# Kernel optimization log

Measured on AMD Instinct MI355X. Metric: run time of the kernel, lower is better.

## Reference

```python
import jax, jax.numpy as jnp
import numpy as np
from jax.scipy.special import logsumexp

B, T, D = 256, 2048, 64


def setup_inputs() -> dict:
    key = jax.random.key(0)
    k1, k2, k3, k4 = jax.random.split(key, 4)
    p = jax.random.normal(k1, (B, T, D), dtype=jnp.float32)
    labels = jax.random.randint(k2, (B, T), 0, D)
    y = jax.nn.one_hot(labels, D, dtype=jnp.int32)  # [B,T,D] one-hot labels
    # valid lengths in [T//2, T]; mask == 1 marks padding positions
    lengths = jax.random.randint(k3, (B,), T // 2, T + 1)
    mask = (jnp.arange(T)[None, :] >= lengths[:, None]).astype(jnp.int32)
    transition = 0.1 * jax.random.normal(k4, (D, D), dtype=jnp.float32)
    return {"p": p, "y": y, "mask": mask, "transition": transition}


def reference(p, y, mask, transition):
    # CRF negative log-likelihood per example: logZ - emission_score - transition_score
    Bb = p.shape[0]
    valid = (1 - mask).astype(jnp.float32)            # [B,T], 1 = valid token
    y1 = y.astype(jnp.float32) * valid[:, :, None]    # masked one-hot labels
    s1 = jnp.sum(y1 * p, axis=(1, 2))                 # emission score
    pair = jnp.einsum('btd,bte->bde', y1[:, :-1], y1[:, 1:])  # label bigram counts
    s2 = jnp.sum(pair * transition, axis=(1, 2))      # transition score

    # forward algorithm: alpha_t = p_t + logsumexp(alpha_{t-1}[:, :, None] + T)
    def step(state, inp):
        new = inp + logsumexp(state[:, :, None] + transition[None, :, :], axis=1)
        return new, new

    xs = jnp.moveaxis(p[:, 1:, :], 1, 0)              # [T-1, B, D]
    _, a1 = jax.lax.scan(step, p[:, 0, :], xs)        # a1: [T-1, B, D]

    # index of alpha at the last valid timestep (length L -> a1 index L-2)
    m1 = jnp.argmin(
        jnp.concatenate([valid.astype(jnp.int32), jnp.zeros((Bb, 1), jnp.int32)], axis=1),
        axis=1) - 2                                   # [B]
    last = a1[m1, jnp.arange(Bb)]                     # [B, D]
    logZ = logsumexp(last, axis=-1)
    return logZ - s1 - s2
```

## Files before the change

### kernel.cpp

```cpp
#include <hip/hip_runtime.h>
#include <stdint.h>
#include <string.h>

#define BB 256
#define TT 2048
#define DD 64
#define CC 64
#define SS 32
#define C_L2E 1.44269504f
#define C_LN2 0.69314718f
#define C_BIAS 0.0028174f

typedef short sh8  __attribute__((ext_vector_type(8)));
typedef float f32x4 __attribute__((ext_vector_type(4)));

union BU { sh8 v8; unsigned int u[4]; unsigned short s[8]; };

__device__ __forceinline__ float expf_fast(float x) { return __builtin_amdgcn_exp2f(x * C_L2E); }
__device__ __forceinline__ unsigned short bf16rne(float x) {
    unsigned int u = __float_as_uint(x);
    u += 0x7FFF + ((u >> 16) & 1u);
    return (unsigned short)(u >> 16);
}
__device__ __forceinline__ unsigned int pkbf(float hi, float lo) {
    return __builtin_amdgcn_perm(__float_as_uint(hi), __float_as_uint(lo), 0x07060302u);
}

#define DPPMAX(x, ctrl, rm, bm) { int _xi = __float_as_int(x);                              \
    int _yi = __builtin_amdgcn_update_dpp(_xi, _xi, ctrl, rm, bm, false);                   \
    x = fmaxf(x, __int_as_float(_yi)); }

__global__ __launch_bounds__(256) void crf_len(
    const int* __restrict__ mask, int* __restrict__ wsL)
{
    __shared__ int r4[4];
    const int c = blockIdx.x, tid = threadIdx.x;
    const int4* mrow = (const int4*)(mask + (size_t)c * TT);
    int4 a = mrow[tid * 2], b = mrow[tid * 2 + 1];
    int s = a.x + a.y + a.z + a.w + b.x + b.y + b.z + b.w;
#pragma unroll
    for (int xm = 32; xm >= 1; xm >>= 1) s += __shfl_xor(s, xm, 64);
    if ((tid & 63) == 0) r4[tid >> 6] = s;
    __syncthreads();
    if (tid == 0) wsL[c] = TT - (r4[0] + r4[1] + r4[2] + r4[3]);
}

__global__ __launch_bounds__(256) void crf_main(
    const float* __restrict__ p, const int* __restrict__ y,
    const int* __restrict__ mask, const float* __restrict__ tr,
    const int* __restrict__ wsL, float* __restrict__ wsS,
    unsigned short* __restrict__ wsA, unsigned short* __restrict__ wsB, int* __restrict__ wsSig)
{
    __shared__ int mk[257];
    __shared__ unsigned char labs[257];
    __shared__ float redf[4];
    const int bid = blockIdx.x;
    const int tid = threadIdx.x;

    if (bid < 512) {
        const int w = tid >> 6, lane = tid & 63;
        const int q = lane >> 4, ml = lane & 15;
        const int cg = bid & 15;
        const int ic = (bid >> 4) * 2 + (w >> 1);
        const int bwd = w & 1;
        const int c = cg * 16 + ml;
        const int Lml = wsL[c];
        const int t0 = ic * SS, t1 = t0 + SS;
        const int ts = (ic == 0) ? 1 : t0;
        const float* prow = p + (size_t)c * TT * DD;

        BU A[4][2];
#pragma unroll
        for (int mt = 0; mt < 4; ++mt)
#pragma unroll
            for (int kt2 = 0; kt2 < 2; ++kt2)
#pragma unroll
                for (int j = 0; j < 8; ++j) {
                    int lam = 32 * kt2 + 16 * (j >> 2) + 4 * q + (j & 3);
                    float tv = bwd ? tr[(16 * mt + ml) * DD + lam] : tr[lam * DD + 16 * mt + ml];
                    A[mt][kt2].s[j] = (short)bf16rne(expf_fast(tv));
                }

        float xs[16];
        if (!bwd && ic == 0) {
#pragma unroll
            for (int k = 0; k < 4; ++k) {
                f32x4 v = *(const f32x4*)(prow + 16 * k + 4 * q);
#pragma unroll
                for (int r = 0; r < 4; ++r)
                    xs[(k >> 1) * 8 + (k & 1) * 4 + r] = __builtin_amdgcn_exp2f(fmaf(v[r], C_L2E, C_BIAS));
            }
        } else {
#pragma unroll
            for (int i = 0; i < 16; ++i) xs[i] = 1.0f;
        }

        int mL = Lml;
#pragma unroll
        for (int xm = 32; xm >= 1; xm >>= 1) { int o = __shfl_xor(mL, xm, 64); mL = o > mL ? o : mL; }
        int ibeg = 0, iend = SS;
        if (!bwd) { int ir = mL - t0; if (ir < 0) ir = 0; iend = (ir + 3) & ~3; if (iend > SS) iend = SS; }
        else      { int ir = t1 - mL; if (ir < 0) ir = 0; ibeg = ir & ~3; if (ibeg > SS) ibeg = SS; }

        int sig = 0;
        const f32x4 z4 = {0.f, 0.f, 0.f, 0.f};

        if (ibeg < iend) {
            f32x4 er[4][4];
#pragma unroll
            for (int s = 0; s < 4; ++s) {
                int i = ibeg + s;
                int t = bwd ? (t1 - 1 - i) : (t0 + i);
#pragma unroll
                for (int k = 0; k < 4; ++k)
                    er[s][k] = *(const f32x4*)(prow + (size_t)t * DD + 16 * k + 4 * q);
            }
            for (int ib = ibeg; ib < iend; ib += 4) {
#pragma unroll
                for (int s = 0; s < 4; ++s) {
                    const int i = ib + s;
                    const int t = bwd ? (t1 - 1 - i) : (t0 + i);
                    const bool act = (t >= ts) && (t < Lml);
                    float ee[4][4];
#pragma unroll
                    for (int k = 0; k < 4; ++k)
#pragma unroll
                        for (int r = 0; r < 4; ++r)
                            ee[k][r] = __builtin_amdgcn_exp2f(fmaf(er[s][k][r], C_L2E, C_BIAS));
                    {
                        int ipf = i + 4;
                        int tpf = bwd ? (t1 - 1 - ipf) : (t0 + ipf);
                        if (tpf < t0) tpf = t0;
                        if (tpf > t1 - 1) tpf = t1 - 1;
#pragma unroll
                        for (int k = 0; k < 4; ++k)
                            er[s][k] = *(const f32x4*)(prow + (size_t)tpf * DD + 16 * k + 4 * q);
                    }
                    float cand[16];
                    BU Bf[2];
                    f32x4 acc[4];
                    if (!bwd) {
#pragma unroll
                        for (int kt2 = 0; kt2 < 2; ++kt2)
#pragma unroll
                            for (int jj = 0; jj < 4; ++jj)
                                Bf[kt2].u[jj] = pkbf(xs[kt2 * 8 + 2 * jj + 1], xs[kt2 * 8 + 2 * jj]);
#pragma unroll
                        for (int mt = 0; mt < 4; ++mt) {
                            acc[mt] = __builtin_amdgcn_mfma_f32_16x16x32_bf16(A[mt][0].v8, Bf[0].v8, z4, 0, 0, 0);
                            acc[mt] = __builtin_amdgcn_mfma_f32_16x16x32_bf16(A[mt][1].v8, Bf[1].v8, acc[mt], 0, 0, 0);
                        }
#pragma unroll
                        for (int mt = 0; mt < 4; ++mt)
#pragma unroll
                            for (int r = 0; r < 4; ++r)
                                cand[(mt >> 1) * 8 + (mt & 1) * 4 + r] = acc[mt][r] * ee[mt][r];
                    } else {
                        float xsc[16];
#pragma unroll
                        for (int kt2 = 0; kt2 < 2; ++kt2)
#pragma unroll
                            for (int h = 0; h < 2; ++h)
#pragma unroll
                                for (int r = 0; r < 4; ++r)
                                    xsc[kt2 * 8 + h * 4 + r] = xs[kt2 * 8 + h * 4 + r] * ee[2 * kt2 + h][r];
#pragma unroll
                        for (int kt2 = 0; kt2 < 2; ++kt2)
#pragma unroll
                            for (int jj = 0; jj < 4; ++jj)
                                Bf[kt2].u[jj] = pkbf(xsc[kt2 * 8 + 2 * jj + 1], xsc[kt2 * 8 + 2 * jj]);
#pragma unroll
                        for (int mt = 0; mt < 4; ++mt) {
                            acc[mt] = __builtin_amdgcn_mfma_f32_16x16x32_bf16(A[mt][0].v8, Bf[0].v8, z4, 0, 0, 0);
                            acc[mt] = __builtin_amdgcn_mfma_f32_16x16x32_bf16(A[mt][1].v8, Bf[1].v8, acc[mt], 0, 0, 0);
                        }
#pragma unroll
                        for (int mt = 0; mt < 4; ++mt)
#pragma unroll
                            for (int r = 0; r < 4; ++r)
                                cand[(mt >> 1) * 8 + (mt & 1) * 4 + r] = acc[mt][r];
                    }
                    if (s == 3) {
                        float mx = fabsf(cand[0]);
#pragma unroll
                        for (int i2 = 1; i2 < 16; ++i2) mx = fmaxf(mx, fabsf(cand[i2]));
                        DPPMAX(mx, 0x111, 0xF, 0xF); DPPMAX(mx, 0x112, 0xF, 0xF);
                        DPPMAX(mx, 0x114, 0xF, 0xF); DPPMAX(mx, 0x118, 0xF, 0xF);
                        DPPMAX(mx, 0x142, 0xA, 0xF); DPPMAX(mx, 0x143, 0xC, 0xF);
                        int smx = __builtin_amdgcn_readlane(__float_as_int(mx), 63);
                        int kk = ((smx >> 23) & 255) - 127;
                        kk = kk < -124 ? -124 : (kk > 124 ? 124 : kk);
                        float sc = __int_as_float((unsigned)(127 - kk) << 23);
#pragma unroll
                        for (int i2 = 0; i2 < 16; ++i2) cand[i2] *= sc;
                        if (act) sig += kk;
                    }
#pragma unroll
                    for (int i2 = 0; i2 < 16; ++i2) xs[i2] = act ? cand[i2] : xs[i2];
                }
            }
        }

        unsigned short* dst = (bwd ? wsB : wsA) + ((size_t)c * CC + ic) * 64;
#pragma unroll
        for (int kt2 = 0; kt2 < 2; ++kt2)
#pragma unroll
            for (int h = 0; h < 2; ++h)
#pragma unroll
                for (int r = 0; r < 4; ++r)
                    dst[32 * kt2 + 16 * h + 4 * q + r] = bf16rne(xs[kt2 * 8 + h * 4 + r]);
        if (!bwd && q == 0) wsSig[c * CC + ic] = sig;

    } else {
        const int sid = bid - 512;
        const int c = sid >> 3, t0 = (sid & 7) * 256;
        const int g = tid & 15, sub = tid >> 4;
        const size_t cb = (size_t)c * TT;

        mk[tid] = mask[cb + t0 + tid];
        if (tid == 0) mk[256] = (t0 + 256 < TT) ? mask[cb + t0 + 256] : 1;
        __syncthreads();

        float s1 = 0.f;
#pragma unroll
        for (int k = 0; k < 16; ++k) {
            const int ti = k * 16 + sub;
            if (mk[ti] == 0) {
                int4 v = ((const int4*)y)[(cb + t0 + ti) * 16 + g];
                int cand = v.w ? 4 * g + 3 : v.z ? 4 * g + 2 : v.y ? 4 * g + 1 : v.x ? 4 * g : -1;
#pragma unroll
                for (int xm = 1; xm <= 8; xm <<= 1) {
                    int o = __shfl_xor(cand, xm, 16);
                    cand = o > cand ? o : cand;
                }
                if (g == 0) {
                    labs[ti] = (unsigned char)cand;
                    s1 += p[(cb + t0 + ti) * DD + cand];
                }
            }
        }
        if (tid < 16 && mk[256] == 0) {
            int4 v = ((const int4*)y)[(cb + t0 + 256) * 16 + tid];
            int cand = v.w ? 4 * tid + 3 : v.z ? 4 * tid + 2 : v.y ? 4 * tid + 1 : v.x ? 4 * tid : -1;
#pragma unroll
            for (int xm = 1; xm <= 8; xm <<= 1) {
                int o = __shfl_xor(cand, xm, 16);
                cand = o > cand ? o : cand;
            }
            if (tid == 0) labs[256] = (unsigned char)cand;
        }
        __syncthreads();

        float s2 = 0.f;
        if (mk[tid + 1] == 0)
            s2 = tr[(int)labs[tid] * DD + (int)labs[tid + 1]];

        float acc = s1 + s2;
#pragma unroll
        for (int xm = 32; xm >= 1; xm >>= 1) acc += __shfl_xor(acc, xm, 64);
        if ((tid & 63) == 0) redf[tid >> 6] = acc;
        __syncthreads();
        if (tid == 0)
            atomicAdd(&wsS[c], redf[0] + redf[1] + redf[2] + redf[3]);
    }
}

__global__ __launch_bounds__(256) void crf_combine(
    const unsigned short* __restrict__ wsA, const unsigned short* __restrict__ wsB,
    const int* __restrict__ wsSig, const float* __restrict__ wsS,
    float* __restrict__ out)
{
    __shared__ float eParts[4];
    const int tid = threadIdx.x, w = tid >> 6, lane = tid & 63;
    const int c = blockIdx.x;

    float Ep = 0.f;
#pragma unroll
    for (int k = 0; k < 16; ++k) {
        const int i = w * 16 + k;
        if (i == 0) continue;
        float b  = __uint_as_float((unsigned)wsB[((size_t)c * CC + i) * 64 + lane] << 16);
        float ap = __uint_as_float((unsigned)wsA[((size_t)c * CC + i - 1) * 64 + lane] << 16);
        float d1 = b * ap, d0 = b;
#pragma unroll
        for (int xm = 32; xm >= 1; xm >>= 1) { d1 += __shfl_xor(d1, xm, 64); d0 += __shfl_xor(d0, xm, 64); }
        Ep += (float)wsSig[c * CC + i] + __builtin_amdgcn_logf(d1) - __builtin_amdgcn_logf(d0);
    }
    if (w == 0) Ep += (float)wsSig[c * CC];
    if (w == 3) {
        float al = __uint_as_float((unsigned)wsA[((size_t)c * CC + CC - 1) * 64 + lane] << 16);
#pragma unroll
        for (int xm = 32; xm >= 1; xm >>= 1) al += __shfl_xor(al, xm, 64);
        Ep += __builtin_amdgcn_logf(al);
    }
    if (lane == 0) eParts[w] = Ep;
    __syncthreads();
    if (tid == 0) {
        float E = eParts[0] + eParts[1] + eParts[2] + eParts[3];
        out[c] = C_LN2 * E - wsS[c];
    }
}

extern "C" void kernel_launch(void* const* d_in, const int* in_sizes, int n_in,
                              void* d_out, int out_size, void* d_ws, size_t ws_size,
                              hipStream_t stream) {
    const float* p  = (const float*)d_in[0];
    const int*   y  = (const int*)d_in[1];
    const int*   mk = (const int*)d_in[2];
    const float* tr = (const float*)d_in[3];
    float* out = (float*)d_out;

    float* wsS  = (float*)d_ws;
    int*   wsL  = (int*)((char*)d_ws + 1024);
    int*   wsSg = (int*)((char*)d_ws + 2048);
    unsigned short* wsA = (unsigned short*)((char*)d_ws + 131072);
    unsigned short* wsB = (unsigned short*)((char*)d_ws + 131072 + (2u << 20));

    hipMemsetAsync(d_ws, 0, 1024, stream);
    crf_len<<<dim3(BB), dim3(256), 0, stream>>>(mk, wsL);
    crf_main<<<dim3(512 + 8 * BB), dim3(256), 0, stream>>>(p, y, mk, tr, wsL, wsS, wsA, wsB, wsSg);
    crf_combine<<<dim3(BB), dim3(256), 0, stream>>>(wsA, wsB, wsSg, wsS, out);
}
```

Baseline: 370.8 us.

## Sort sequences by length so forward groups skip padded chunks, split score kernel

Adds a single-block rank kernel that sorts the batch by valid length and uses the permutation to group 16 similar-length sequences per block in the chunked forward/backward kernel. Because each wave trims its loop to the maximum length in its group, grouping similar lengths lets more chunks be skipped. The emission/transition score work is split into its own kernel rather than sharing one grid with the recurrence. This adds an extra serial launch and a tiny ranking kernel, and loses the overlap of score blocks with the recurrence blocks.

```diff
diff --git a/kernel.cpp b/kernel.cpp
--- a/kernel.cpp
+++ b/kernel.cpp
@@ -45,224 +45,240 @@
     if (tid == 0) wsL[c] = TT - (r4[0] + r4[1] + r4[2] + r4[3]);
 }
 
-__global__ __launch_bounds__(256) void crf_main(
+__global__ __launch_bounds__(256) void crf_rank(
+    const int* __restrict__ wsL, int* __restrict__ perm)
+{
+    __shared__ int Ls[BB];
+    const int tid = threadIdx.x;
+    Ls[tid] = wsL[tid];
+    __syncthreads();
+    const int L = Ls[tid];
+    int r = 0;
+#pragma unroll 8
+    for (int j = 0; j < BB; ++j) {
+        int Lj = Ls[j];
+        r += (Lj < L) || (Lj == L && j < tid);
+    }
+    perm[r] = tid;
+}
+
+__global__ __launch_bounds__(256) void crf_score(
     const float* __restrict__ p, const int* __restrict__ y,
     const int* __restrict__ mask, const float* __restrict__ tr,
-    const int* __restrict__ wsL, float* __restrict__ wsS,
-    unsigned short* __restrict__ wsA, unsigned short* __restrict__ wsB, int* __restrict__ wsSig)
+    float* __restrict__ wsS)
 {
     __shared__ int mk[257];
     __shared__ unsigned char labs[257];
     __shared__ float redf[4];
-    const int bid = blockIdx.x;
+    const int c = blockIdx.y, t0 = blockIdx.x * 256;
     const int tid = threadIdx.x;
-
-    if (bid < 512) {
-        const int w = tid >> 6, lane = tid & 63;
-        const int q = lane >> 4, ml = lane & 15;
-        const int cg = bid & 15;
-        const int ic = (bid >> 4) * 2 + (w >> 1);
-        const int bwd = w & 1;
-        const int c = cg * 16 + ml;
-        const int Lml = wsL[c];
-        const int t0 = ic * SS, t1 = t0 + SS;
-        const int ts = (ic == 0) ? 1 : t0;
-        const float* prow = p + (size_t)c * TT * DD;
-
-        BU A[4][2];
-#pragma unroll
-        for (int mt = 0; mt < 4; ++mt)
-#pragma unroll
-            for (int kt2 = 0; kt2 < 2; ++kt2)
-#pragma unroll
-                for (int j = 0; j < 8; ++j) {
-                    int lam = 32 * kt2 + 16 * (j >> 2) + 4 * q + (j & 3);
-                    float tv = bwd ? tr[(16 * mt + ml) * DD + lam] : tr[lam * DD + 16 * mt + ml];
-                    A[mt][kt2].s[j] = (short)bf16rne(expf_fast(tv));
-                }
-
-        float xs[16];
-        if (!bwd && ic == 0) {
-#pragma unroll
-            for (int k = 0; k < 4; ++k) {
-                f32x4 v = *(const f32x4*)(prow + 16 * k + 4 * q);
-#pragma unroll
-                for (int r = 0; r < 4; ++r)
-                    xs[(k >> 1) * 8 + (k & 1) * 4 + r] = __builtin_amdgcn_exp2f(fmaf(v[r], C_L2E, C_BIAS));
-            }
-        } else {
-#pragma unroll
-            for (int i = 0; i < 16; ++i) xs[i] = 1.0f;
-        }
-
-        int mL = Lml;
-#pragma unroll
-        for (int xm = 32; xm >= 1; xm >>= 1) { int o = __shfl_xor(mL, xm, 64); mL = o > mL ? o : mL; }
-        int ibeg = 0, iend = SS;
-        if (!bwd) { int ir = mL - t0; if (ir < 0) ir = 0; iend = (ir + 3) & ~3; if (iend > SS) iend = SS; }
-        else      { int ir = t1 - mL; if (ir < 0) ir = 0; ibeg = ir & ~3; if (ibeg > SS) ibeg = SS; }
-
-        int sig = 0;
-        const f32x4 z4 = {0.f, 0.f, 0.f, 0.f};
-
-        if (ibeg < iend) {
-            f32x4 er[4][4];
-#pragma unroll
-            for (int s = 0; s < 4; ++s) {
-                int i = ibeg + s;
-                int t = bwd ? (t1 - 1 - i) : (t0 + i);
-#pragma unroll
-                for (int k = 0; k < 4; ++k)
-                    er[s][k] = *(const f32x4*)(prow + (size_t)t * DD + 16 * k + 4 * q);
-            }
-            for (int ib = ibeg; ib < iend; ib += 4) {
-#pragma unroll
-                for (int s = 0; s < 4; ++s) {
-                    const int i = ib + s;
-                    const int t = bwd ? (t1 - 1 - i) : (t0 + i);
-                    const bool act = (t >= ts) && (t < Lml);
-                    float ee[4][4];
-#pragma unroll
-                    for (int k = 0; k < 4; ++k)
-#pragma unroll
-                        for (int r = 0; r < 4; ++r)
-                            ee[k][r] = __builtin_amdgcn_exp2f(fmaf(er[s][k][r], C_L2E, C_BIAS));
-                    {
-                        int ipf = i + 4;
-                        int tpf = bwd ? (t1 - 1 - ipf) : (t0 + ipf);
-                        if (tpf < t0) tpf = t0;
-                        if (tpf > t1 - 1) tpf = t1 - 1;
-#pragma unroll
-                        for (int k = 0; k < 4; ++k)
-                            er[s][k] = *(const f32x4*)(prow + (size_t)tpf * DD + 16 * k + 4 * q);
-                    }
-                    float cand[16];
-                    BU Bf[2];
-                    f32x4 acc[4];
-                    if (!bwd) {
-#pragma unroll
-                        for (int kt2 = 0; kt2 < 2; ++kt2)
-#pragma unroll
-                            for (int jj = 0; jj < 4; ++jj)
-                                Bf[kt2].u[jj] = pkbf(xs[kt2 * 8 + 2 * jj + 1], xs[kt2 * 8 + 2 * jj]);
-#pragma unroll
-                        for (int mt = 0; mt < 4; ++mt) {
-                            acc[mt] = __builtin_amdgcn_mfma_f32_16x16x32_bf16(A[mt][0].v8, Bf[0].v8, z4, 0, 0, 0);
-                            acc[mt] = __builtin_amdgcn_mfma_f32_16x16x32_bf16(A[mt][1].v8, Bf[1].v8, acc[mt], 0, 0, 0);
-                        }
-#pragma unroll
-                        for (int mt = 0; mt < 4; ++mt)
-#pragma unroll
-                            for (int r = 0; r < 4; ++r)
-                                cand[(mt >> 1) * 8 + (mt & 1) * 4 + r] = acc[mt][r] * ee[mt][r];
-                    } else {
-                        float xsc[16];
-#pragma unroll
-                        for (int kt2 = 0; kt2 < 2; ++kt2)
-#pragma unroll
-                            for (int h = 0; h < 2; ++h)
-#pragma unroll
-                                for (int r = 0; r < 4; ++r)
-                                    xsc[kt2 * 8 + h * 4 + r] = xs[kt2 * 8 + h * 4 + r] * ee[2 * kt2 + h][r];
-#pragma unroll
-                        for (int kt2 = 0; kt2 < 2; ++kt2)
-#pragma unroll
-                            for (int jj = 0; jj < 4; ++jj)
-                                Bf[kt2].u[jj] = pkbf(xsc[kt2 * 8 + 2 * jj + 1], xsc[kt2 * 8 + 2 * jj]);
-#pragma unroll
-                        for (int mt = 0; mt < 4; ++mt) {
-                            acc[mt] = __builtin_amdgcn_mfma_f32_16x16x32_bf16(A[mt][0].v8, Bf[0].v8, z4, 0, 0, 0);
-                            acc[mt] = __builtin_amdgcn_mfma_f32_16x16x32_bf16(A[mt][1].v8, Bf[1].v8, acc[mt], 0, 0, 0);
-                        }
-#pragma unroll
-                        for (int mt = 0; mt < 4; ++mt)
-#pragma unroll
-                            for (int r = 0; r < 4; ++r)
-                                cand[(mt >> 1) * 8 + (mt & 1) * 4 + r] = acc[mt][r];
-                    }
-                    if (s == 3) {
-                        float mx = fabsf(cand[0]);
-#pragma unroll
-                        for (int i2 = 1; i2 < 16; ++i2) mx = fmaxf(mx, fabsf(cand[i2]));
-                        DPPMAX(mx, 0x111, 0xF, 0xF); DPPMAX(mx, 0x112, 0xF, 0xF);
-                        DPPMAX(mx, 0x114, 0xF, 0xF); DPPMAX(mx, 0x118, 0xF, 0xF);
-                        DPPMAX(mx, 0x142, 0xA, 0xF); DPPMAX(mx, 0x143, 0xC, 0xF);
-                        int smx = __builtin_amdgcn_readlane(__float_as_int(mx), 63);
-                        int kk = ((smx >> 23) & 255) - 127;
-                        kk = kk < -124 ? -124 : (kk > 124 ? 124 : kk);
-                        float sc = __int_as_float((unsigned)(127 - kk) << 23);
-#pragma unroll
-                        for (int i2 = 0; i2 < 16; ++i2) cand[i2] *= sc;
-                        if (act) sig += kk;
-                    }
-#pragma unroll
-                    for (int i2 = 0; i2 < 16; ++i2) xs[i2] = act ? cand[i2] : xs[i2];
-                }
-            }
-        }
-
-        unsigned short* dst = (bwd ? wsB : wsA) + ((size_t)c * CC + ic) * 64;
-#pragma unroll
-        for (int kt2 = 0; kt2 < 2; ++kt2)
-#pragma unroll
-            for (int h = 0; h < 2; ++h)
-#pragma unroll
-                for (int r = 0; r < 4; ++r)
-                    dst[32 * kt2 + 16 * h + 4 * q + r] = bf16rne(xs[kt2 * 8 + h * 4 + r]);
-        if (!bwd && q == 0) wsSig[c * CC + ic] = sig;
-
-    } else {
-        const int sid = bid - 512;
-        const int c = sid >> 3, t0 = (sid & 7) * 256;
-        const int g = tid & 15, sub = tid >> 4;
-        const size_t cb = (size_t)c * TT;
-
-        mk[tid] = mask[cb + t0 + tid];
-        if (tid == 0) mk[256] = (t0 + 256 < TT) ? mask[cb + t0 + 256] : 1;
-        __syncthreads();
-
-        float s1 = 0.f;
-#pragma unroll
-        for (int k = 0; k < 16; ++k) {
-            const int ti = k * 16 + sub;
-            if (mk[ti] == 0) {
-                int4 v = ((const int4*)y)[(cb + t0 + ti) * 16 + g];
-                int cand = v.w ? 4 * g + 3 : v.z ? 4 * g + 2 : v.y ? 4 * g + 1 : v.x ? 4 * g : -1;
-#pragma unroll
-                for (int xm = 1; xm <= 8; xm <<= 1) {
-                    int o = __shfl_xor(cand, xm, 16);
-                    cand = o > cand ? o : cand;
-                }
-                if (g == 0) {
-                    labs[ti] = (unsigned char)cand;
-                    s1 += p[(cb + t0 + ti) * DD + cand];
-                }
-            }
-        }
-        if (tid < 16 && mk[256] == 0) {
-            int4 v = ((const int4*)y)[(cb + t0 + 256) * 16 + tid];
-            int cand = v.w ? 4 * tid + 3 : v.z ? 4 * tid + 2 : v.y ? 4 * tid + 1 : v.x ? 4 * tid : -1;
+    const int g = tid & 15, sub = tid >> 4;
+    const size_t cb = (size_t)c * TT;
+
+    mk[tid] = mask[cb + t0 + tid];
+    if (tid == 0) mk[256] = (t0 + 256 < TT) ? mask[cb + t0 + 256] : 1;
+    __syncthreads();
+
+    float s1 = 0.f;
+#pragma unroll
+    for (int k = 0; k < 16; ++k) {
+        const int ti = k * 16 + sub;
+        if (mk[ti] == 0) {
+            int4 v = ((const int4*)y)[(cb + t0 + ti) * 16 + g];
+            int cand = v.w ? 4 * g + 3 : v.z ? 4 * g + 2 : v.y ? 4 * g + 1 : v.x ? 4 * g : -1;
 #pragma unroll
             for (int xm = 1; xm <= 8; xm <<= 1) {
                 int o = __shfl_xor(cand, xm, 16);
                 cand = o > cand ? o : cand;
             }
-            if (tid == 0) labs[256] = (unsigned char)cand;
-        }
-        __syncthreads();
-
-        float s2 = 0.f;
-        if (mk[tid + 1] == 0)
-            s2 = tr[(int)labs[tid] * DD + (int)labs[tid + 1]];
-
-        float acc = s1 + s2;
-#pragma unroll
-        for (int xm = 32; xm >= 1; xm >>= 1) acc += __shfl_xor(acc, xm, 64);
-        if ((tid & 63) == 0) redf[tid >> 6] = acc;
-        __syncthreads();
-        if (tid == 0)
-            atomicAdd(&wsS[c], redf[0] + redf[1] + redf[2] + redf[3]);
-    }
+            if (g == 0) {
+                labs[ti] = (unsigned char)cand;
+                s1 += p[(cb + t0 + ti) * DD + cand];
+            }
+        }
+    }
+    if (tid < 16 && mk[256] == 0) {
+        int4 v = ((const int4*)y)[(cb + t0 + 256) * 16 + tid];
+        int cand = v.w ? 4 * tid + 3 : v.z ? 4 * tid + 2 : v.y ? 4 * tid + 1 : v.x ? 4 * tid : -1;
+#pragma unroll
+        for (int xm = 1; xm <= 8; xm <<= 1) {
+            int o = __shfl_xor(cand, xm, 16);
+            cand = o > cand ? o : cand;
+        }
+        if (tid == 0) labs[256] = (unsigned char)cand;
+    }
+    __syncthreads();
+
+    float s2 = 0.f;
+    if (mk[tid + 1] == 0)
+        s2 = tr[(int)labs[tid] * DD + (int)labs[tid + 1]];
+
+    float acc = s1 + s2;
+#pragma unroll
+    for (int xm = 32; xm >= 1; xm >>= 1) acc += __shfl_xor(acc, xm, 64);
+    if ((tid & 63) == 0) redf[tid >> 6] = acc;
+    __syncthreads();
+    if (tid == 0)
+        atomicAdd(&wsS[c], redf[0] + redf[1] + redf[2] + redf[3]);
+}
+
+__global__ __launch_bounds__(256) void crf_probe(
+    const float* __restrict__ p, const float* __restrict__ tr,
+    const int* __restrict__ wsL, const int* __restrict__ perm,
+    unsigned short* __restrict__ wsA, unsigned short* __restrict__ wsB, int* __restrict__ wsSig)
+{
+    const int tid = threadIdx.x, w = tid >> 6, lane = tid & 63;
+    const int q = lane >> 4, ml = lane & 15;
+    const int cg = blockIdx.x;
+    const int ic = blockIdx.y * 2 + (w >> 1);
+    const int bwd = w & 1;
+    const int c = perm[cg * 16 + ml];
+    const int Lml = wsL[c];
+    const int t0 = ic * SS, t1 = t0 + SS;
+    const int ts = (ic == 0) ? 1 : t0;
+    const float* prow = p + (size_t)c * TT * DD;
+
+    BU A[4][2];
+#pragma unroll
+    for (int mt = 0; mt < 4; ++mt)
+#pragma unroll
+        for (int kt2 = 0; kt2 < 2; ++kt2)
+#pragma unroll
+            for (int j = 0; j < 8; ++j) {
+                int lam = 32 * kt2 + 16 * (j >> 2) + 4 * q + (j & 3);
+                float tv = bwd ? tr[(16 * mt + ml) * DD + lam] : tr[lam * DD + 16 * mt + ml];
+                A[mt][kt2].s[j] = (short)bf16rne(expf_fast(tv));
+            }
+
+    float xs[16];
+    if (!bwd && ic == 0) {
+#pragma unroll
+        for (int k = 0; k < 4; ++k) {
+            f32x4 v = *(const f32x4*)(prow + 16 * k + 4 * q);
+#pragma unroll
+            for (int r = 0; r < 4; ++r)
+                xs[(k >> 1) * 8 + (k & 1) * 4 + r] = __builtin_amdgcn_exp2f(fmaf(v[r], C_L2E, C_BIAS));
+        }
+    } else {
+#pragma unroll
+        for (int i = 0; i < 16; ++i) xs[i] = 1.0f;
+    }
+
+    int mL = Lml;
+#pragma unroll
+    for (int xm = 32; xm >= 1; xm >>= 1) { int o = __shfl_xor(mL, xm, 64); mL = o > mL ? o : mL; }
+    int ibeg = 0, iend = SS;
+    if (!bwd) { int ir = mL - t0; if (ir < 0) ir = 0; iend = (ir + 3) & ~3; if (iend > SS) iend = SS; }
+    else      { int ir = t1 - mL; if (ir < 0) ir = 0; ibeg = ir & ~3; if (ibeg > SS) ibeg = SS; }
+
+    int sig = 0;
+    const f32x4 z4 = {0.f, 0.f, 0.f, 0.f};
+
+    if (ibeg < iend) {
+        f32x4 er[4][4];
+#pragma unroll
+        for (int s = 0; s < 4; ++s) {
+            int i = ibeg + s;
+            int t = bwd ? (t1 - 1 - i) : (t0 + i);
+#pragma unroll
+            for (int k = 0; k < 4; ++k)
+                er[s][k] = *(const f32x4*)(prow + (size_t)t * DD + 16 * k + 4 * q);
+        }
+        for (int ib = ibeg; ib < iend; ib += 4) {
+#pragma unroll
+            for (int s = 0; s < 4; ++s) {
+                const int i = ib + s;
+                const int t = bwd ? (t1 - 1 - i) : (t0 + i);
+                const bool act = (t >= ts) && (t < Lml);
+                float ee[4][4];
+#pragma unroll
+                for (int k = 0; k < 4; ++k)
+#pragma unroll
+                    for (int r = 0; r < 4; ++r)
+                        ee[k][r] = __builtin_amdgcn_exp2f(fmaf(er[s][k][r], C_L2E, C_BIAS));
+                {
+                    int ipf = i + 4;
+                    int tpf = bwd ? (t1 - 1 - ipf) : (t0 + ipf);
+                    if (tpf < t0) tpf = t0;
+                    if (tpf > t1 - 1) tpf = t1 - 1;
+#pragma unroll
+                    for (int k = 0; k < 4; ++k)
+                        er[s][k] = *(const f32x4*)(prow + (size_t)tpf * DD + 16 * k + 4 * q);
+                }
+                float cand[16];
+                BU Bf[2];
+                f32x4 acc[4];
+                if (!bwd) {
+#pragma unroll
+                    for (int kt2 = 0; kt2 < 2; ++kt2)
+#pragma unroll
+                        for (int jj = 0; jj < 4; ++jj)
+                            Bf[kt2].u[jj] = pkbf(xs[kt2 * 8 + 2 * jj + 1], xs[kt2 * 8 + 2 * jj]);
+#pragma unroll
+                    for (int mt = 0; mt < 4; ++mt) {
+                        acc[mt] = __builtin_amdgcn_mfma_f32_16x16x32_bf16(A[mt][0].v8, Bf[0].v8, z4, 0, 0, 0);
+                        acc[mt] = __builtin_amdgcn_mfma_f32_16x16x32_bf16(A[mt][1].v8, Bf[1].v8, acc[mt], 0, 0, 0);
+                    }
+#pragma unroll
+                    for (int mt = 0; mt < 4; ++mt)
+#pragma unroll
+                        for (int r = 0; r < 4; ++r)
+                            cand[(mt >> 1) * 8 + (mt & 1) * 4 + r] = acc[mt][r] * ee[mt][r];
+                } else {
+                    float xsc[16];
+#pragma unroll
+                    for (int kt2 = 0; kt2 < 2; ++kt2)
+#pragma unroll
+                        for (int h = 0; h < 2; ++h)
+#pragma unroll
+                            for (int r = 0; r < 4; ++r)
+                                xsc[kt2 * 8 + h * 4 + r] = xs[kt2 * 8 + h * 4 + r] * ee[2 * kt2 + h][r];
+#pragma unroll
+                    for (int kt2 = 0; kt2 < 2; ++kt2)
+#pragma unroll
+                        for (int jj = 0; jj < 4; ++jj)
+                            Bf[kt2].u[jj] = pkbf(xsc[kt2 * 8 + 2 * jj + 1], xsc[kt2 * 8 + 2 * jj]);
+#pragma unroll
+                    for (int mt = 0; mt < 4; ++mt) {
+                        acc[mt] = __builtin_amdgcn_mfma_f32_16x16x32_bf16(A[mt][0].v8, Bf[0].v8, z4, 0, 0, 0);
+                        acc[mt] = __builtin_amdgcn_mfma_f32_16x16x32_bf16(A[mt][1].v8, Bf[1].v8, acc[mt], 0, 0, 0);
+                    }
+#pragma unroll
+                    for (int mt = 0; mt < 4; ++mt)
+#pragma unroll
+                        for (int r = 0; r < 4; ++r)
+                            cand[(mt >> 1) * 8 + (mt & 1) * 4 + r] = acc[mt][r];
+                }
+                if (s == 3) {
+                    float mx = fabsf(cand[0]);
+#pragma unroll
+                    for (int i2 = 1; i2 < 16; ++i2) mx = fmaxf(mx, fabsf(cand[i2]));
+                    DPPMAX(mx, 0x111, 0xF, 0xF); DPPMAX(mx, 0x112, 0xF, 0xF);
+                    DPPMAX(mx, 0x114, 0xF, 0xF); DPPMAX(mx, 0x118, 0xF, 0xF);
+                    DPPMAX(mx, 0x142, 0xA, 0xF); DPPMAX(mx, 0x143, 0xC, 0xF);
+                    int smx = __builtin_amdgcn_readlane(__float_as_int(mx), 63);
+                    int kk = ((smx >> 23) & 255) - 127;
+                    kk = kk < -124 ? -124 : (kk > 124 ? 124 : kk);
+                    float sc = __int_as_float((unsigned)(127 - kk) << 23);
+#pragma unroll
+                    for (int i2 = 0; i2 < 16; ++i2) cand[i2] *= sc;
+                    if (act) sig += kk;
+                }
+#pragma unroll
+                for (int i2 = 0; i2 < 16; ++i2) xs[i2] = act ? cand[i2] : xs[i2];
+            }
+        }
+    }
+
+    unsigned short* dst = (bwd ? wsB : wsA) + ((size_t)c * CC + ic) * 64;
+#pragma unroll
+    for (int kt2 = 0; kt2 < 2; ++kt2)
+#pragma unroll
+        for (int h = 0; h < 2; ++h)
+#pragma unroll
+            for (int r = 0; r < 4; ++r)
+                dst[32 * kt2 + 16 * h + 4 * q + r] = bf16rne(xs[kt2 * 8 + h * 4 + r]);
+    if (!bwd && q == 0) wsSig[c * CC + ic] = sig;
 }
 
 __global__ __launch_bounds__(256) void crf_combine(
@@ -312,12 +328,15 @@
 
     float* wsS  = (float*)d_ws;
     int*   wsL  = (int*)((char*)d_ws + 1024);
-    int*   wsSg = (int*)((char*)d_ws + 2048);
+    int*   wsPm = (int*)((char*)d_ws + 2048);
+    int*   wsSg = (int*)((char*)d_ws + 4096);
     unsigned short* wsA = (unsigned short*)((char*)d_ws + 131072);
     unsigned short* wsB = (unsigned short*)((char*)d_ws + 131072 + (2u << 20));
 
     hipMemsetAsync(d_ws, 0, 1024, stream);
     crf_len<<<dim3(BB), dim3(256), 0, stream>>>(mk, wsL);
-    crf_main<<<dim3(512 + 8 * BB), dim3(256), 0, stream>>>(p, y, mk, tr, wsL, wsS, wsA, wsB, wsSg);
+    crf_rank<<<dim3(1), dim3(256), 0, stream>>>(wsL, wsPm);
+    crf_score<<<dim3(8, BB), dim3(256), 0, stream>>>(p, y, mk, tr, wsS);
+    crf_probe<<<dim3(16, CC / 2), dim3(256), 0, stream>>>(p, tr, wsL, wsPm, wsA, wsB, wsSg);
     crf_combine<<<dim3(BB), dim3(256), 0, stream>>>(wsA, wsB, wsSg, wsS, out);
 }
```

Result: faster. 324.3 us (-12.5%).
